# Kernel optimization log

Hardware: AMD Instinct MI355X
Metric: run time of the kernel (lower is better)

The kernel has to match this reference:

```python
import jax, jax.numpy as jnp
import numpy as np

EPS = 1e-12
N = 8192
D_LOW = 2


def setup_inputs() -> dict:
    key = jax.random.key(0)
    k1, k2 = jax.random.split(key)
    # High-dim affinity distribution: strictly positive, sums to 1 (t-SNE P matrix)
    u = jax.random.uniform(k1, (N, N), dtype=jnp.float32, minval=0.1, maxval=1.0)
    P = u / u.sum()
    # Learned low-dim embedding (nn.Embedding(n, d).weight)
    Y = jax.random.normal(k2, (N, D_LOW), dtype=jnp.float32)
    dof = 1  # Student-t degrees of freedom (standard t-SNE)
    return {"P": P, "Y": Y, "dof": dof}


def reference(P, Y, dof):
    # Pairwise squared Euclidean distances: D[i,j] = ||Y_i - Y_j||^2
    Y2 = jnp.sum(Y * Y, axis=1, keepdims=True)          # (n, 1)
    Dm = Y2 - 2.0 * (Y @ Y.T) + Y2.T                     # (n, n)
    # Student-t affinities with zeroed diagonal
    Q = (1.0 + Dm / dof) ** (-(dof + 1) / 2.0)
    Q = Q.at[jnp.diag_indices(Q.shape[0])].set(0.0)
    # Global normalization + clamp
    Q = jnp.clip(Q / jnp.sum(Q), EPS)
    # KL(P || Q)  (metric == 'kl' branch)
    return jnp.sum(P * jnp.log(P / Q))
```

## Files before the change

kernel.cpp:

```cpp
#include <hip/hip_runtime.h>


static constexpr int N_PTS  = 8192;
static constexpr int TPB    = 256;
static constexpr int RS4    = N_PTS / 4;
static constexpr int CT     = N_PTS / (TPB * 4);
static constexpr int RPB    = 32;
static constexpr int RT     = N_PTS / RPB;
static constexpr int NBATCH = RPB / 4;

__global__ __launch_bounds__(TPB, 4) void kl_partial_kernel(
    const float* __restrict__ P, const float* __restrict__ Y,
    double* __restrict__ ws)
{
    const int bid  = blockIdx.x;
    const int ct   = bid & (CT - 1);
    const int rt   = bid >> 3;
    const int colq = ct * TPB + threadIdx.x;
    const int rowbase = rt * RPB;

    const float4* __restrict__ Y4 = reinterpret_cast<const float4*>(Y);
    const float4 ya = Y4[2 * colq];
    const float4 yb = Y4[2 * colq + 1];
    const float jx[4] = {ya.x, ya.z, yb.x, yb.z};
    const float jy[4] = {ya.y, ya.w, yb.y, yb.w};

    __shared__ float2 yis[RPB];
    if (threadIdx.x < RPB)
        yis[threadIdx.x] = reinterpret_cast<const float2*>(Y)[rowbase + threadIdx.x];
    __syncthreads();

    const float4* __restrict__ Pq =
        reinterpret_cast<const float4*>(P) + (size_t)rowbase * RS4 + colq;

    float sA[4] = {0.f, 0.f, 0.f, 0.f};
    float sB[4] = {0.f, 0.f, 0.f, 0.f};
    float sS[4] = {0.f, 0.f, 0.f, 0.f};

    auto compute = [&](int s, const float4 p, float yix, float yiy) {
        const float pv[4] = {p.x, p.y, p.z, p.w};
#pragma unroll
        for (int k = 0; k < 4; ++k) {
            float dx  = yix - jx[k];
            float dy  = yiy - jy[k];
            float opd = __builtin_fmaf(dy, dy, __builtin_fmaf(dx, dx, 1.0f));
            sA[s] = __builtin_fmaf(pv[k], __log2f(pv[k] * opd), sA[s]);
            sS[s] += __builtin_amdgcn_rcpf(opd);
            sB[s] += pv[k];
        }
    };

    float4 a0 = Pq[0 * RS4], a1 = Pq[1 * RS4], a2 = Pq[2 * RS4], a3 = Pq[3 * RS4];
    Pq += (size_t)4 * RS4;

#pragma unroll
    for (int b = 0; b < NBATCH; ++b) {
        float4 n0, n1, n2, n3;
        if (b + 1 < NBATCH) {
            n0 = Pq[0 * RS4]; n1 = Pq[1 * RS4]; n2 = Pq[2 * RS4]; n3 = Pq[3 * RS4];
            Pq += (size_t)4 * RS4;
        }
        const float2 yi0 = yis[4 * b + 0];
        const float2 yi1 = yis[4 * b + 1];
        const float2 yi2 = yis[4 * b + 2];
        const float2 yi3 = yis[4 * b + 3];
        compute(0, a0, yi0.x, yi0.y);
        compute(1, a1, yi1.x, yi1.y);
        compute(2, a2, yi2.x, yi2.y);
        compute(3, a3, yi3.x, yi3.y);
        if (b + 1 < NBATCH) { a0 = n0; a1 = n1; a2 = n2; a3 = n3; }
    }

    double dA = (double)((sA[0] + sA[1]) + (sA[2] + sA[3]));
    double dB = (double)((sB[0] + sB[1]) + (sB[2] + sB[3]));
    double dS = (double)((sS[0] + sS[1]) + (sS[2] + sS[3]));

#pragma unroll
    for (int off = 32; off > 0; off >>= 1) {
        dA += __shfl_down(dA, off);
        dB += __shfl_down(dB, off);
        dS += __shfl_down(dS, off);
    }

    __shared__ double red[4][3];
    const int wave = threadIdx.x >> 6, lane = threadIdx.x & 63;
    if (lane == 0) { red[wave][0] = dA; red[wave][1] = dB; red[wave][2] = dS; }
    __syncthreads();
    if (threadIdx.x == 0) {
        double a = (red[0][0] + red[1][0]) + (red[2][0] + red[3][0]);
        double b = (red[0][1] + red[1][1]) + (red[2][1] + red[3][1]);
        double s = (red[0][2] + red[1][2]) + (red[2][2] + red[3][2]);
        atomicAdd(&ws[0], a);
        atomicAdd(&ws[1], b);
        atomicAdd(&ws[2], s);
    }
}

__global__ __launch_bounds__(TPB) void kl_final_kernel(
    const float* __restrict__ P, const double* __restrict__ ws,
    float* __restrict__ out)
{
    const int t = threadIdx.x;
    double tr = 0.0;
    for (int i = t; i < N_PTS; i += TPB)
        tr += (double)P[(size_t)i * (N_PTS + 1)];

#pragma unroll
    for (int off = 32; off > 0; off >>= 1)
        tr += __shfl_down(tr, off);

    __shared__ double red[4];
    if ((t & 63) == 0) red[t >> 6] = tr;
    __syncthreads();
    if (t == 0) {
        const double trace = red[0] + red[1] + red[2] + red[3];
        const double A2 = ws[0], B = ws[1], S = ws[2];
        const double LN2     = 0.6931471805599453;
        const double LOG_EPS = -27.631021115928547;
        double kl = LN2 * A2 + (B - trace) * log(S - (double)N_PTS)
                  - trace * LOG_EPS;
        out[0] = (float)kl;
    }
}

extern "C" void kernel_launch(void* const* d_in, const int* in_sizes, int n_in,
                              void* d_out, int out_size, void* d_ws, size_t ws_size,
                              hipStream_t stream) {
    const float* P = (const float*)d_in[0];
    const float* Y = (const float*)d_in[1];
    double* ws = (double*)d_ws;

    hipMemsetAsync(d_ws, 0, 3 * sizeof(double), stream);

    hipLaunchKernelGGL(kl_partial_kernel, dim3(CT * RT), dim3(TPB), 0, stream,
                       P, Y, ws);
    hipLaunchKernelGGL(kl_final_kernel, dim3(1), dim3(TPB), 0, stream,
                       P, ws, (float*)d_out);
}
```

Baseline: 393.2 us.

## Deepen P prefetch and replace global atomics with per-block partial sums

Result: faster. 369.0 us (-6.1%).

```diff
diff --git a/kernel.cpp b/kernel.cpp
--- a/kernel.cpp
+++ b/kernel.cpp
@@ -7,6 +7,7 @@
 static constexpr int CT     = N_PTS / (TPB * 4);
 static constexpr int RPB    = 32;
 static constexpr int RT     = N_PTS / RPB;
+static constexpr int NBLK   = CT * RT;
 static constexpr int NBATCH = RPB / 4;
 
 __global__ __launch_bounds__(TPB, 4) void kl_partial_kernel(
@@ -50,13 +51,15 @@
         }
     };
 
-    float4 a0 = Pq[0 * RS4], a1 = Pq[1 * RS4], a2 = Pq[2 * RS4], a3 = Pq[3 * RS4];
+    float4 c0 = Pq[0 * RS4], c1 = Pq[1 * RS4], c2 = Pq[2 * RS4], c3 = Pq[3 * RS4];
+    Pq += (size_t)4 * RS4;
+    float4 e0 = Pq[0 * RS4], e1 = Pq[1 * RS4], e2 = Pq[2 * RS4], e3 = Pq[3 * RS4];
     Pq += (size_t)4 * RS4;
 
 #pragma unroll
     for (int b = 0; b < NBATCH; ++b) {
         float4 n0, n1, n2, n3;
-        if (b + 1 < NBATCH) {
+        if (b + 2 < NBATCH) {
             n0 = Pq[0 * RS4]; n1 = Pq[1 * RS4]; n2 = Pq[2 * RS4]; n3 = Pq[3 * RS4];
             Pq += (size_t)4 * RS4;
         }
@@ -64,11 +67,12 @@
         const float2 yi1 = yis[4 * b + 1];
         const float2 yi2 = yis[4 * b + 2];
         const float2 yi3 = yis[4 * b + 3];
-        compute(0, a0, yi0.x, yi0.y);
-        compute(1, a1, yi1.x, yi1.y);
-        compute(2, a2, yi2.x, yi2.y);
-        compute(3, a3, yi3.x, yi3.y);
-        if (b + 1 < NBATCH) { a0 = n0; a1 = n1; a2 = n2; a3 = n3; }
+        compute(0, c0, yi0.x, yi0.y);
+        compute(1, c1, yi1.x, yi1.y);
+        compute(2, c2, yi2.x, yi2.y);
+        compute(3, c3, yi3.x, yi3.y);
+        c0 = e0; c1 = e1; c2 = e2; c3 = e3;
+        if (b + 2 < NBATCH) { e0 = n0; e1 = n1; e2 = n2; e3 = n3; }
     }
 
     double dA = (double)((sA[0] + sA[1]) + (sA[2] + sA[3]));
@@ -87,12 +91,9 @@
     if (lane == 0) { red[wave][0] = dA; red[wave][1] = dB; red[wave][2] = dS; }
     __syncthreads();
     if (threadIdx.x == 0) {
-        double a = (red[0][0] + red[1][0]) + (red[2][0] + red[3][0]);
-        double b = (red[0][1] + red[1][1]) + (red[2][1] + red[3][1]);
-        double s = (red[0][2] + red[1][2]) + (red[2][2] + red[3][2]);
-        atomicAdd(&ws[0], a);
-        atomicAdd(&ws[1], b);
-        atomicAdd(&ws[2], s);
+        ws[3 * bid + 0] = (red[0][0] + red[1][0]) + (red[2][0] + red[3][0]);
+        ws[3 * bid + 1] = (red[0][1] + red[1][1]) + (red[2][1] + red[3][1]);
+        ws[3 * bid + 2] = (red[0][2] + red[1][2]) + (red[2][2] + red[3][2]);
     }
 }
 
@@ -101,20 +102,43 @@
     float* __restrict__ out)
 {
     const int t = threadIdx.x;
+
+    float trv[N_PTS / TPB];
+#pragma unroll
+    for (int u = 0; u < N_PTS / TPB; ++u)
+        trv[u] = P[(size_t)(t + u * TPB) * (N_PTS + 1)];
     double tr = 0.0;
-    for (int i = t; i < N_PTS; i += TPB)
-        tr += (double)P[(size_t)i * (N_PTS + 1)];
+#pragma unroll
+    for (int u = 0; u < N_PTS / TPB; ++u) tr += (double)trv[u];
+
+    double a = 0.0, b = 0.0, s = 0.0;
+#pragma unroll
+    for (int u = 0; u < NBLK / TPB; ++u) {
+        const int idx = t + u * TPB;
+        a += ws[3 * idx + 0];
+        b += ws[3 * idx + 1];
+        s += ws[3 * idx + 2];
+    }
 
 #pragma unroll
-    for (int off = 32; off > 0; off >>= 1)
+    for (int off = 32; off > 0; off >>= 1) {
         tr += __shfl_down(tr, off);
+        a  += __shfl_down(a,  off);
+        b  += __shfl_down(b,  off);
+        s  += __shfl_down(s,  off);
+    }
 
-    __shared__ double red[4];
-    if ((t & 63) == 0) red[t >> 6] = tr;
+    __shared__ double red[4][4];
+    if ((t & 63) == 0) {
+        red[t >> 6][0] = tr; red[t >> 6][1] = a;
+        red[t >> 6][2] = b;  red[t >> 6][3] = s;
+    }
     __syncthreads();
     if (t == 0) {
-        const double trace = red[0] + red[1] + red[2] + red[3];
-        const double A2 = ws[0], B = ws[1], S = ws[2];
+        double trace = red[0][0] + red[1][0] + red[2][0] + red[3][0];
+        double A2    = red[0][1] + red[1][1] + red[2][1] + red[3][1];
+        double B     = red[0][2] + red[1][2] + red[2][2] + red[3][2];
+        double S     = red[0][3] + red[1][3] + red[2][3] + red[3][3];
         const double LN2     = 0.6931471805599453;
         const double LOG_EPS = -27.631021115928547;
         double kl = LN2 * A2 + (B - trace) * log(S - (double)N_PTS)
@@ -130,9 +154,7 @@
     const float* Y = (const float*)d_in[1];
     double* ws = (double*)d_ws;
 
-    hipMemsetAsync(d_ws, 0, 3 * sizeof(double), stream);
-
-    hipLaunchKernelGGL(kl_partial_kernel, dim3(CT * RT), dim3(TPB), 0, stream,
+    hipLaunchKernelGGL(kl_partial_kernel, dim3(NBLK), dim3(TPB), 0, stream,
                        P, Y, ws);
     hipLaunchKernelGGL(kl_final_kernel, dim3(1), dim3(TPB), 0, stream,
                        P, ws, (float*)d_out);
```
